# Kernel tuning notes

Measured on AMD Instinct MI355X. Metric: run time of the kernel, lower is better.

The kernel has to match this reference:

```python
import jax, jax.numpy as jnp
import numpy as np

HEAD = 64            # RWKV_HEAD_SIZE
C = 1024             # n_embd = dim_att
F = 4096             # dim_ffn
B, T = 8, 256
H = C // HEAD
N_LAYER, LAYER_ID = 12, 1
GN_EPS = 1e-5 * 8 ** 2   # GroupNorm eps = 1e-5 * head_size_divisor^2


def bshift(x):
    """bidirectional_shift_multihead: per head, first half of channels shifted
    forward in time (right), second half shifted backward (left), zero-padded."""
    b, t, c = x.shape
    x4 = x.reshape(b, t, c // HEAD, HEAD)
    mid = HEAD // 2
    f = jnp.pad(x4[:, :-1, :, :mid], ((0, 0), (1, 0), (0, 0), (0, 0)))
    r = jnp.pad(x4[:, 1:, :, mid:], ((0, 0), (0, 1), (0, 0), (0, 0)))
    return jnp.concatenate([f, r], -1).reshape(b, t, c)


def layernorm(x, g, b):
    m = jnp.mean(x, -1, keepdims=True)
    v = jnp.mean((x - m) ** 2, -1, keepdims=True)
    return (x - m) * jax.lax.rsqrt(v + 1e-5) * g + b


def groupnorm(x, g, b):
    bb, t, c = x.shape
    xg = x.reshape(bb, t, H, HEAD)
    m = jnp.mean(xg, -1, keepdims=True)
    v = jnp.mean((xg - m) ** 2, -1, keepdims=True)
    return ((xg - m) * jax.lax.rsqrt(v + GN_EPS)).reshape(bb, t, c) * g + b


def wkv6_bi(r, k, v, w, u):
    """Bidirectional WKV6. r,k,v,w: [B,T,H,N]; u: [H,N].
    y_t = r_t . (S^fwd_t + u*k_t v_t^T + S^bwd_t), with per-channel decay
    d_t = exp(-exp(w_t)) applied to the state after each step in each direction."""
    d = jnp.exp(-jnp.exp(w))
    rT, kT, vT, dT = (jnp.moveaxis(a, 1, 0) for a in (r, k, v, d))  # [T,B,H,N]
    S0 = jnp.zeros((B, H, HEAD, HEAD), r.dtype)
    uB = u[None]  # [1,H,N]

    def fstep(S, inp):
        rt, kt, vt, dt = inp
        kv = kt[..., None] * vt[..., None, :]              # [B,H,N,N]
        y = jnp.einsum('bhj,bhji->bhi', rt, S + uB[..., None] * kv)
        return dt[..., None] * S + kv, y

    _, yf = jax.lax.scan(fstep, S0, (rT, kT, vT, dT))

    def bstep(S, inp):
        rt, kt, vt, dt = inp
        y = jnp.einsum('bhj,bhji->bhi', rt, S)
        return dt[..., None] * S + kt[..., None] * vt[..., None, :], y

    _, yb = jax.lax.scan(bstep, S0, (rT, kT, vT, dT), reverse=True)
    return jnp.moveaxis(yf + yb, 0, 1)  # [B,T,H,N]


def block_forward(x, ln1_g, ln1_b, ln2_g, ln2_b,
                  maa_x, maa_w, maa_k, maa_v, maa_r, maa_g, maa_w1, maa_w2,
                  time_decay, tdw1, tdw2, u, Wr, Wk, Wv, Wg, Wo, lnx_g, lnx_b,
                  cmaa_k, cmaa_r, Wck, Wcv, Wcr):
    # ---- RWKV_Tmix_V6 (attention) branch ----
    xa = layernorm(x, ln1_g, ln1_b)
    xx = bshift(xa) - xa
    a = jnp.tanh((xa + xx * maa_x) @ maa_w1).reshape(B, T, 5, -1)   # [B,T,5,32]
    m = jnp.einsum('btfd,fdc->fbtc', a, maa_w2)                      # [5,B,T,C]
    xw = xa + xx * (maa_w + m[0])
    xk = xa + xx * (maa_k + m[1])
    xv = xa + xx * (maa_v + m[2])
    xr = xa + xx * (maa_r + m[3])
    xg = xa + xx * (maa_g + m[4])
    r = (xr @ Wr).reshape(B, T, H, HEAD)
    k = (xk @ Wk).reshape(B, T, H, HEAD)
    v = (xv @ Wv).reshape(B, T, H, HEAD)
    g = jax.nn.silu(xg @ Wg)
    w = (time_decay + jnp.tanh(xw @ tdw1) @ tdw2).reshape(B, T, H, HEAD)
    y = wkv6_bi(r, k, v, w, u).reshape(B, T, C)
    y = groupnorm(y, lnx_g, lnx_b)
    x = x + (y * g) @ Wo
    # ---- RWKV_CMix_V6 (FFN) branch ----
    xc = layernorm(x, ln2_g, ln2_b)
    cxx = bshift(xc) - xc
    kk = jnp.square(jax.nn.relu((xc + cxx * cmaa_k) @ Wck))
    kv = kk @ Wcv
    x = x + jax.nn.sigmoid((xc + cxx * cmaa_r) @ Wcr) * kv
    return x


def setup_inputs() -> dict:
    key = jax.random.key(0)
    ks = jax.random.split(key, 16)
    r1 = 1.0 - LAYER_ID / N_LAYER            # ratio_1_to_almost0
    r0 = LAYER_ID / (N_LAYER - 1)            # ratio_0_to_1
    ddd = np.arange(C, dtype=np.float64) / C
    base = (1.0 - ddd ** r1).astype(np.float32)
    half = (1.0 - ddd ** (0.5 * r1)).astype(np.float32)
    s = 0.02
    p = {}
    p['x'] = jax.random.normal(ks[0], (B, T, C), jnp.float32)
    p['ln1_g'] = jnp.ones((C,), jnp.float32)
    p['ln1_b'] = jnp.zeros((C,), jnp.float32)
    p['ln2_g'] = jnp.ones((C,), jnp.float32)
    p['ln2_b'] = jnp.zeros((C,), jnp.float32)
    p['maa_x'] = jnp.asarray(base)
    p['maa_w'] = jnp.asarray(base)
    p['maa_k'] = jnp.asarray(base)
    p['maa_v'] = jnp.asarray((1.0 - (ddd ** r1 + 0.3 * r0)).astype(np.float32))
    p['maa_r'] = jnp.asarray(half)
    p['maa_g'] = jnp.asarray(half)
    p['maa_w1'] = jax.random.uniform(ks[1], (C, 160), jnp.float32, -0.01, 0.01)
    p['maa_w2'] = jax.random.uniform(ks[2], (5, 32, C), jnp.float32, -0.01, 0.01)
    n = np.arange(C, dtype=np.float64)
    p['time_decay'] = jnp.asarray((-6.0 + 5.0 * (n / (C - 1)) ** (0.7 + 1.3 * r0)).astype(np.float32))
    p['tdw1'] = jax.random.uniform(ks[3], (C, 64), jnp.float32, -0.01, 0.01)
    p['tdw2'] = jax.random.uniform(ks[4], (64, C), jnp.float32, -0.01, 0.01)
    faaaa = r0 * (1.0 - n / (C - 1)) + ((n + 1) % 3 - 1) * 0.1
    p['u'] = jnp.asarray(faaaa.reshape(H, HEAD).astype(np.float32))
    p['Wr'] = jax.random.normal(ks[5], (C, C), jnp.float32) * s
    p['Wk'] = jax.random.normal(ks[6], (C, C), jnp.float32) * s
    p['Wv'] = jax.random.normal(ks[7], (C, C), jnp.float32) * s
    p['Wg'] = jax.random.normal(ks[8], (C, C), jnp.float32) * s
    p['Wo'] = jax.random.normal(ks[9], (C, C), jnp.float32) * s
    p['lnx_g'] = jnp.ones((C,), jnp.float32)
    p['lnx_b'] = jnp.zeros((C,), jnp.float32)
    p['cmaa_k'] = jnp.asarray(base)
    p['cmaa_r'] = jnp.asarray(base)
    p['Wck'] = jax.random.normal(ks[10], (C, F), jnp.float32) * s
    p['Wcv'] = jax.random.normal(ks[11], (F, C), jnp.float32) * s
    p['Wcr'] = jax.random.normal(ks[12], (C, C), jnp.float32) * s
    return p


def reference(x, ln1_g, ln1_b, ln2_g, ln2_b,
              maa_x, maa_w, maa_k, maa_v, maa_r, maa_g, maa_w1, maa_w2,
              time_decay, tdw1, tdw2, u, Wr, Wk, Wv, Wg, Wo, lnx_g, lnx_b,
              cmaa_k, cmaa_r, Wck, Wcv, Wcr):
    return block_forward(x, ln1_g, ln1_b, ln2_g, ln2_b,
                         maa_x, maa_w, maa_k, maa_v, maa_r, maa_g, maa_w1, maa_w2,
                         time_decay, tdw1, tdw2, u, Wr, Wk, Wv, Wg, Wo, lnx_g, lnx_b,
                         cmaa_k, cmaa_r, Wck, Wcv, Wcr)
```

## Files before the change

### kernel.cpp

```cpp
#include <hip/hip_runtime.h>
#include <math.h>
#include <stdint.h>

static constexpr int B  = 8;
static constexpr int T  = 256;
static constexpr int C  = 1024;
static constexpr int H  = 16;
static constexpr int HEAD = 64;
static constexpr int FF = 4096;
static constexpr int BT = B * T;
static constexpr int NCH = 8;
static constexpr int CS  = 32;

typedef short short8  __attribute__((ext_vector_type(8)));
typedef float floatx4 __attribute__((ext_vector_type(4)));

__device__ __forceinline__ float bf2f(ushort u) {
    return __uint_as_float(((uint32_t)u) << 16);
}
__device__ __forceinline__ ushort f2bf(float x) {
    uint32_t u = __float_as_uint(x);
    u += 0x7fff + ((u >> 16) & 1);
    return (ushort)(u >> 16);
}

__device__ __forceinline__ void gload16(const void* g, void* l) {
    __builtin_amdgcn_global_load_lds(
        (const __attribute__((address_space(1))) unsigned int*)g,
        (__attribute__((address_space(3))) unsigned int*)l, 16, 0, 0);
}

#define BEPI_NONE_BF   0
#define BEPI_SILU_BF   1
#define BEPI_RELUSQ_BF 2
#define BEPI_NONE_F    3
#define BEPI_RES_F     4
#define BEPI_SIGRES_F  5
#define BEPI_TANH_F    6
#define BEPI_TANH_BF   7
#define BEPI_DECAY_F   8
#define BEPI_SIGRES2_F 9

__device__ __forceinline__ void red6(float (&vals)[6], float* red)
{
    const int wave = threadIdx.x >> 6, lane = threadIdx.x & 63;
#pragma unroll
    for (int i = 0; i < 6; ++i) {
        float v = vals[i];
#pragma unroll
        for (int off = 32; off > 0; off >>= 1) v += __shfl_xor(v, off);
        if (lane == 0) red[i * 4 + wave] = v;
    }
    __syncthreads();
#pragma unroll
    for (int i = 0; i < 6; ++i)
        vals[i] = red[i * 4 + 0] + red[i * 4 + 1] + red[i * 4 + 2] + red[i * 4 + 3];
}

__global__ __launch_bounds__(256) void lnshiftmix_kernel(const float* __restrict__ x,
                                                         const float* __restrict__ g,
                                                         const float* __restrict__ b,
                                                         const float* __restrict__ maa,
                                                         float* __restrict__ xa,
                                                         float* __restrict__ xx,
                                                         ushort* __restrict__ ax)
{
    const int row = blockIdx.x;
    const int t = row & (T - 1);
    const int tid = threadIdx.x;
    __shared__ float red[24];
    const float4 vc = reinterpret_cast<const float4*>(x + (size_t)row * C)[tid];
    float4 vp = make_float4(0.f, 0.f, 0.f, 0.f), vn = make_float4(0.f, 0.f, 0.f, 0.f);
    if (t > 0)     vp = reinterpret_cast<const float4*>(x + (size_t)(row - 1) * C)[tid];
    if (t < T - 1) vn = reinterpret_cast<const float4*>(x + (size_t)(row + 1) * C)[tid];
    float vals[6];
    vals[0] = vc.x + vc.y + vc.z + vc.w;
    vals[1] = vc.x * vc.x + vc.y * vc.y + vc.z * vc.z + vc.w * vc.w;
    vals[2] = vp.x + vp.y + vp.z + vp.w;
    vals[3] = vp.x * vp.x + vp.y * vp.y + vp.z * vp.z + vp.w * vp.w;
    vals[4] = vn.x + vn.y + vn.z + vn.w;
    vals[5] = vn.x * vn.x + vn.y * vn.y + vn.z * vn.z + vn.w * vn.w;
    red6(vals, red);
    const float mc = vals[0] * (1.f / C);
    const float rc = rsqrtf(fmaxf(vals[1] * (1.f / C) - mc * mc, 0.f) + 1e-5f);
    const float mp = vals[2] * (1.f / C);
    const float rp = rsqrtf(fmaxf(vals[3] * (1.f / C) - mp * mp, 0.f) + 1e-5f);
    const float mn = vals[4] * (1.f / C);
    const float rn = rsqrtf(fmaxf(vals[5] * (1.f / C) - mn * mn, 0.f) + 1e-5f);

    const int c = tid * 4;
    const bool fh = ((c & 63) < 32);
    const float cur[4] = {vc.x, vc.y, vc.z, vc.w};
    const float nbr[4] = {fh ? vp.x : vn.x, fh ? vp.y : vn.y,
                          fh ? vp.z : vn.z, fh ? vp.w : vn.w};
    const float mN = fh ? mp : mn, rN = fh ? rp : rn;
    const bool nvalid = fh ? (t > 0) : (t < T - 1);
    const size_t rb = (size_t)row * C;
#pragma unroll
    for (int e = 0; e < 4; ++e) {
        const float gg = g[c + e], bb = b[c + e];
        const float av = (cur[e] - mc) * rc * gg + bb;
        const float sv = nvalid ? ((nbr[e] - mN) * rN * gg + bb) : 0.f;
        const float xv = sv - av;
        xa[rb + c + e] = av;
        xx[rb + c + e] = xv;
        ax[rb + c + e] = f2bf(av + xv * maa[c + e]);
    }
}

__global__ __launch_bounds__(256) void lnshiftcmix_kernel(const float* __restrict__ x,
                                                          const float* __restrict__ g,
                                                          const float* __restrict__ b,
                                                          const float* __restrict__ mk,
                                                          const float* __restrict__ mr,
                                                          ushort* __restrict__ ok,
                                                          ushort* __restrict__ orr)
{
    const int row = blockIdx.x;
    const int t = row & (T - 1);
    const int tid = threadIdx.x;
    __shared__ float red[24];
    const float4 vc = reinterpret_cast<const float4*>(x + (size_t)row * C)[tid];
    float4 vp = make_float4(0.f, 0.f, 0.f, 0.f), vn = make_float4(0.f, 0.f, 0.f, 0.f);
    if (t > 0)     vp = reinterpret_cast<const float4*>(x + (size_t)(row - 1) * C)[tid];
    if (t < T - 1) vn = reinterpret_cast<const float4*>(x + (size_t)(row + 1) * C)[tid];
    float vals[6];
    vals[0] = vc.x + vc.y + vc.z + vc.w;
    vals[1] = vc.x * vc.x + vc.y * vc.y + vc.z * vc.z + vc.w * vc.w;
    vals[2] = vp.x + vp.y + vp.z + vp.w;
    vals[3] = vp.x * vp.x + vp.y * vp.y + vp.z * vp.z + vp.w * vp.w;
    vals[4] = vn.x + vn.y + vn.z + vn.w;
    vals[5] = vn.x * vn.x + vn.y * vn.y + vn.z * vn.z + vn.w * vn.w;
    red6(vals, red);
    const float mc = vals[0] * (1.f / C);
    const float rc = rsqrtf(fmaxf(vals[1] * (1.f / C) - mc * mc, 0.f) + 1e-5f);
    const float mp = vals[2] * (1.f / C);
    const float rp = rsqrtf(fmaxf(vals[3] * (1.f / C) - mp * mp, 0.f) + 1e-5f);
    const float mn = vals[4] * (1.f / C);
    const float rn = rsqrtf(fmaxf(vals[5] * (1.f / C) - mn * mn, 0.f) + 1e-5f);

    const int c = tid * 4;
    const bool fh = ((c & 63) < 32);
    const float cur[4] = {vc.x, vc.y, vc.z, vc.w};
    const float nbr[4] = {fh ? vp.x : vn.x, fh ? vp.y : vn.y,
                          fh ? vp.z : vn.z, fh ? vp.w : vn.w};
    const float mN = fh ? mp : mn, rN = fh ? rp : rn;
    const bool nvalid = fh ? (t > 0) : (t < T - 1);
    const size_t rb = (size_t)row * C;
#pragma unroll
    for (int e = 0; e < 4; ++e) {
        const float gg = g[c + e], bb = b[c + e];
        const float av = (cur[e] - mc) * rc * gg + bb;
        const float sv = nvalid ? ((nbr[e] - mN) * rN * gg + bb) : 0.f;
        const float xv = sv - av;
        ok[rb + c + e]  = f2bf(av + xv * mk[c + e]);
        orr[rb + c + e] = f2bf(av + xv * mr[c + e]);
    }
}

__global__ __launch_bounds__(1024) void gnmul_kernel(const ushort* __restrict__ yf,
                                                     const ushort* __restrict__ yb,
                                                     const float* __restrict__ g,
                                                     const float* __restrict__ b,
                                                     const ushort* __restrict__ gate,
                                                     const ushort* __restrict__ vin,
                                                     const ushort* __restrict__ rbuf,
                                                     const ushort* __restrict__ kbuf,
                                                     const float* __restrict__ u,
                                                     ushort* __restrict__ out)
{
    const int row = blockIdx.x;
    const int tid = threadIdx.x;
    const size_t idx = (size_t)row * C + tid;
    float p = bf2f(rbuf[idx]) * bf2f(kbuf[idx]) * u[tid];
#pragma unroll
    for (int off = 32; off > 0; off >>= 1) p += __shfl_xor(p, off);
    const float v = bf2f(yf[idx]) + bf2f(yb[idx]) + p * bf2f(vin[idx]);
    float s = v;
#pragma unroll
    for (int off = 32; off > 0; off >>= 1) s += __shfl_xor(s, off);
    const float m = s * (1.0f / HEAD);
    const float d = v - m;
    float q = d * d;
#pragma unroll
    for (int off = 32; off > 0; off >>= 1) q += __shfl_xor(q, off);
    const float rstd = rsqrtf(q * (1.0f / HEAD) + 6.4e-4f);
    out[idx] = f2bf((d * rstd * g[tid] + b[tid]) * bf2f(gate[idx]));
}

struct WJobs {
    const float* W[8];
    ushort* dst[8];
    int Kd[8], Nd[8], ntx[8], base[8];
    int njobs;
};
__global__ __launch_bounds__(256) void wconvB_kernel(WJobs jobs)
{
    __shared__ float tile[32][33];
    const int bid = blockIdx.x;
    int j = 0;
#pragma unroll
    for (int i = 1; i < 8; ++i)
        if (i < jobs.njobs && bid >= jobs.base[i]) j = i;
    const float* __restrict__ W = jobs.W[j];
    ushort* __restrict__ dst = jobs.dst[j];
    const int Kd = jobs.Kd[j], Nd = jobs.Nd[j];
    const int local = bid - jobs.base[j];
    const int n0 = (local % jobs.ntx[j]) * 32;
    const int k0 = (local / jobs.ntx[j]) * 32;
    const int tx = threadIdx.x, ty = threadIdx.y;
#pragma unroll
    for (int i = 0; i < 4; ++i)
        tile[ty * 4 + i][tx] = W[(size_t)(k0 + ty * 4 + i) * Nd + n0 + tx];
    __syncthreads();
#pragma unroll
    for (int i = 0; i < 4; ++i)
        dst[(size_t)(n0 + ty * 4 + i) * Kd + k0 + tx] = f2bf(tile[tx][ty * 4 + i]);
}

__global__ __launch_bounds__(256) void wconv_kernel(const float* __restrict__ W,
                                                    ushort* __restrict__ Wt,
                                                    int Kd, int Nd)
{
    __shared__ float tile[32][33];
    const int n0 = blockIdx.x * 32, k0 = blockIdx.y * 32;
    const int tx = threadIdx.x, ty = threadIdx.y;
#pragma unroll
    for (int i = 0; i < 4; ++i)
        tile[ty * 4 + i][tx] = W[(size_t)(k0 + ty * 4 + i) * Nd + n0 + tx];
    __syncthreads();
#pragma unroll
    for (int i = 0; i < 4; ++i)
        Wt[(size_t)(n0 + ty * 4 + i) * Kd + k0 + tx] = f2bf(tile[tx][ty * 4 + i]);
}

struct Wconv4Args { const float* W[4]; };
__global__ __launch_bounds__(256) void wconv4_kernel(Wconv4Args args, ushort* __restrict__ Wt)
{
    __shared__ float tile[32][33];
    const int z = blockIdx.z;
    const float* __restrict__ W = args.W[z];
    ushort* __restrict__ dst = Wt + (size_t)z * C * C;
    const int n0 = blockIdx.x * 32, k0 = blockIdx.y * 32;
    const int tx = threadIdx.x, ty = threadIdx.y;
#pragma unroll
    for (int i = 0; i < 4; ++i)
        tile[ty * 4 + i][tx] = W[(size_t)(k0 + ty * 4 + i) * C + n0 + tx];
    __syncthreads();
#pragma unroll
    for (int i = 0; i < 4; ++i)
        dst[(size_t)(n0 + ty * 4 + i) * C + k0 + tx] = f2bf(tile[tx][ty * 4 + i]);
}

struct Mix5Args { const float* maa[5]; ushort* out[5]; };
__global__ __launch_bounds__(256) void mix5m_kernel(const ushort* __restrict__ a5b,
                                                    const ushort* __restrict__ w2t,
                                                    const float* __restrict__ xa,
                                                    const float* __restrict__ xx,
                                                    Mix5Args args)
{
    __shared__ __align__(16) ushort As[128 * 32];
    __shared__ __align__(16) ushort Bs[64 * 32];
    const int f = blockIdx.z;
    const int bm = blockIdx.y * 128, bn = blockIdx.x * 64;
    const int tid = threadIdx.x;
    const int wid = tid >> 6, lane = tid & 63;
    const int wr = wid >> 1, wc = wid & 1;
    const int l15 = lane & 15, lhi = lane >> 4;

#pragma unroll
    for (int p = 0; p < 2; ++p) {
        const int lin = p * 256 + tid;
        const int row = lin >> 2;
        const int sp = (lin & 3) ^ ((row >> 1) & 3);
        gload16(a5b + (size_t)(bm + row) * 160 + f * 32 + sp * 8, &As[lin * 8]);
    }
    {
        const int lin = tid;
        const int n = lin >> 2;
        const int sp = (lin & 3) ^ ((n >> 1) & 3);
        gload16(w2t + ((size_t)f * C + bn + n) * 32 + sp * 8, &Bs[lin * 8]);
    }
    __syncthreads();

    short8 af[4], bfr[2];
#pragma unroll
    for (int m = 0; m < 4; ++m) {
        const int row = wr * 64 + m * 16 + l15;
        const int sp = lhi ^ ((row >> 1) & 3);
        af[m] = *(const short8*)&As[row * 32 + sp * 8];
    }
#pragma unroll
    for (int n = 0; n < 2; ++n) {
        const int col = wc * 32 + n * 16 + l15;
        const int sp = lhi ^ ((col >> 1) & 3);
        bfr[n] = *(const short8*)&Bs[col * 32 + sp * 8];
    }
    floatx4 acc[4][2];
#pragma unroll
    for (int m = 0; m < 4; ++m)
#pragma unroll
        for (int n = 0; n < 2; ++n)
            acc[m][n] = __builtin_amdgcn_mfma_f32_16x16x32_bf16(
                af[m], bfr[n], (floatx4){0.f, 0.f, 0.f, 0.f}, 0, 0, 0);

    const float* __restrict__ maa = args.maa[f];
    ushort* __restrict__ out = args.out[f];
#pragma unroll
    for (int m = 0; m < 4; ++m) {
        const int row0 = bm + wr * 64 + m * 16 + lhi * 4;
#pragma unroll
        for (int n = 0; n < 2; ++n) {
            const int col = bn + wc * 32 + n * 16 + l15;
            const float mc = maa[col];
#pragma unroll
            for (int j = 0; j < 4; ++j) {
                const size_t oi = (size_t)(row0 + j) * C + col;
                out[oi] = f2bf(xa[oi] + xx[oi] * (mc + acc[m][n][j]));
            }
        }
    }
}

__global__ __launch_bounds__(256) void wkv_pass1(const ushort* __restrict__ k,
                                                 const ushort* __restrict__ v,
                                                 const float* __restrict__ d,
                                                 ushort* __restrict__ M,
                                                 float* __restrict__ D)
{
    const int uc = blockIdx.x;
    const int c = uc & (NCH - 1), unit = uc >> 3;
    const int dir = unit & 1, bh = unit >> 1;
    const int tid = threadIdx.x;
    const int wv = tid >> 6, lane = tid & 63;
    const int l15 = lane & 15, lhi = lane >> 4;
    const size_t rowb = ((size_t)(bh >> 4) * T * H + (bh & 15)) * HEAD;
    const int s0 = c * CS;

    __shared__ ushort kT[64][40];
    __shared__ ushort vt[64][40];
    __shared__ float  Ldd[CS][64];

    for (int idx = tid; idx < CS * 64; idx += 256) {
        const int s = idx >> 6, j = idx & 63;
        const int t = dir ? (T - 1 - (s0 + s)) : (s0 + s);
        const size_t g = rowb + (size_t)t * (H * HEAD) + j;
        kT[j][s] = k[g];
        vt[j][s] = v[g];
        Ldd[s][j] = d[g];
    }
    __syncthreads();

    if (tid < 64) {
        const int j = tid;
        float G = 1.f;
#pragma unroll
        for (int s = CS - 1; s >= 0; --s) {
            kT[j][s] = f2bf(bf2f(kT[j][s]) * G);
            G *= Ldd[s][j];
        }
        D[(size_t)uc * 64 + j] = G;
    }
    __syncthreads();

    const short8 av = *(const short8*)&vt[wv * 16 + l15][lhi * 8];
    ushort* __restrict__ mrow = M + (size_t)uc * 4096;
#pragma unroll
    for (int n = 0; n < 4; ++n) {
        const short8 bk = *(const short8*)&kT[n * 16 + l15][lhi * 8];
        const floatx4 acc = __builtin_amdgcn_mfma_f32_16x16x32_bf16(
            av, bk, (floatx4){0.f, 0.f, 0.f, 0.f}, 0, 0, 0);
#pragma unroll
        for (int jr = 0; jr < 4; ++jr) {
            const int i = wv * 16 + lhi * 4 + jr;
            mrow[(size_t)i * 64 + n * 16 + l15] = f2bf(acc[jr]);
        }
    }
}

__global__ __launch_bounds__(1024) void wkv_pass2(ushort* __restrict__ M,
                                                  const float* __restrict__ D)
{
    const int unit = blockIdx.x;
    const int tid = threadIdx.x;
    const int j0 = (tid & 15) * 4;
    float S0 = 0.f, S1 = 0.f, S2 = 0.f, S3 = 0.f;
#pragma unroll
    for (int c = 0; c < NCH; ++c) {
        const int uc = unit * NCH + c;
        const float4 Dv = *reinterpret_cast<const float4*>(D + (size_t)uc * 64 + j0);
        ushort* mp = M + (size_t)uc * 4096 + tid * 4;
        const uint2 mv = *reinterpret_cast<const uint2*>(mp);
        const float m0 = bf2f((ushort)(mv.x & 0xffff));
        const float m1 = bf2f((ushort)(mv.x >> 16));
        const float m2 = bf2f((ushort)(mv.y & 0xffff));
        const float m3 = bf2f((ushort)(mv.y >> 16));
        uint2 sv;
        sv.x = (uint32_t)f2bf(S0) | ((uint32_t)f2bf(S1) << 16);
        sv.y = (uint32_t)f2bf(S2) | ((uint32_t)f2bf(S3) << 16);
        *reinterpret_cast<uint2*>(mp) = sv;
        S0 = fmaf(Dv.x, S0, m0);
        S1 = fmaf(Dv.y, S1, m1);
        S2 = fmaf(Dv.z, S2, m2);
        S3 = fmaf(Dv.w, S3, m3);
    }
}

__global__ __launch_bounds__(256) void wkv_ymfma(const ushort* __restrict__ r,
                                                 const ushort* __restrict__ k,
                                                 const ushort* __restrict__ v,
                                                 const float* __restrict__ d,
                                                 const ushort* __restrict__ Sin,
                                                 ushort* __restrict__ yf,
                                                 ushort* __restrict__ yb)
{
    const int uc = blockIdx.x;
    const int c = uc & (NCH - 1), unit = uc >> 3;
    const int dir = unit & 1, bh = unit >> 1;
    const int tid = threadIdx.x;
    const int wv = tid >> 6, lane = tid & 63;
    const int l15 = lane & 15, lhi = lane >> 4;
    const size_t rowb = ((size_t)(bh >> 4) * T * H + (bh & 15)) * HEAD;
    const int s0 = c * CS;

    __shared__ ushort rp[32][64];
    __shared__ ushort kp[32][64];
    __shared__ ushort vt[64][40];
    __shared__ ushort Pl[32][32];
    __shared__ float  Ldd[CS][64];

    for (int idx = tid; idx < 32 * 64; idx += 256) {
        const int s = idx >> 6, j = idx & 63;
        const int t = dir ? (T - 1 - (s0 + s)) : (s0 + s);
        const size_t g = rowb + (size_t)t * (H * HEAD) + j;
        const int cs = (j >> 3) ^ (s & 7);
        rp[s][cs * 8 + (j & 7)] = r[g];
        kp[s][cs * 8 + (j & 7)] = k[g];
        vt[j][s] = v[g];
        Ldd[s][j] = d[g];
    }
    __syncthreads();

    if (wv == 0) {
        const int j = lane;
        float Q = 1.f;
#pragma unroll
        for (int s = 0; s < 32; ++s) {
            const int a = ((j >> 3) ^ (s & 7)) * 8 + (j & 7);
            rp[s][a] = f2bf(bf2f(rp[s][a]) * Q);
            Q *= Ldd[s][j];
        }
    } else if (wv == 1) {
        const int j = lane;
        float iQ = 1.f;
#pragma unroll
        for (int s = 0; s < 32; ++s) {
            iQ *= (1.0f / Ldd[s][j]);
            const int a = ((j >> 3) ^ (s & 7)) * 8 + (j & 7);
            kp[s][a] = f2bf(bf2f(kp[s][a]) * iQ);
        }
    }
    __syncthreads();

    const int st = wv & 1;
    const int ip = wv >> 1;

    short8 ar[2];
#pragma unroll
    for (int ks = 0; ks < 2; ++ks) {
        const int row = st * 16 + l15;
        const int ch = (ks * 4 + lhi) ^ (row & 7);
        ar[ks] = *(const short8*)&rp[row][ch * 8];
    }

    floatx4 acc[2];
#pragma unroll
    for (int n = 0; n < 2; ++n) {
        const int i = ip * 32 + n * 16 + l15;
        const ushort* sp = Sin + (size_t)uc * 4096 + (size_t)i * 64;
        const short8 b0 = *(const short8*)&sp[lhi * 8];
        const short8 b1 = *(const short8*)&sp[32 + lhi * 8];
        acc[n] = __builtin_amdgcn_mfma_f32_16x16x32_bf16(ar[0], b0, (floatx4){0.f, 0.f, 0.f, 0.f}, 0, 0, 0);
        acc[n] = __builtin_amdgcn_mfma_f32_16x16x32_bf16(ar[1], b1, acc[n], 0, 0, 0);
    }

    if (wv < 2) {
#pragma unroll
        for (int ut = 0; ut < 2; ++ut) {
            const int urow = ut * 16 + l15;
            const short8 bk0 = *(const short8*)&kp[urow][((0 + lhi) ^ (urow & 7)) * 8];
            const short8 bk1 = *(const short8*)&kp[urow][((4 + lhi) ^ (urow & 7)) * 8];
            floatx4 pa = __builtin_amdgcn_mfma_f32_16x16x32_bf16(ar[0], bk0, (floatx4){0.f, 0.f, 0.f, 0.f}, 0, 0, 0);
            pa = __builtin_amdgcn_mfma_f32_16x16x32_bf16(ar[1], bk1, pa, 0, 0, 0);
            const int sg0 = st * 16 + lhi * 4;
            const int ug = ut * 16 + l15;
#pragma unroll
            for (int jr = 0; jr < 4; ++jr) {
                const float val = (ug < sg0 + jr) ? pa[jr] : 0.f;
                Pl[sg0 + jr][ug] = f2bf(val);
            }
        }
    }
    __syncthreads();

    short8 ap;
    {
        const int row = st * 16 + l15;
        ap = *(const short8*)&Pl[row][lhi * 8];
    }
#pragma unroll
    for (int n = 0; n < 2; ++n) {
        const int i = ip * 32 + n * 16 + l15;
        const short8 bv = *(const short8*)&vt[i][lhi * 8];
        acc[n] = __builtin_amdgcn_mfma_f32_16x16x32_bf16(ap, bv, acc[n], 0, 0, 0);
    }

    ushort* __restrict__ yo = dir ? yb : yf;
#pragma unroll
    for (int n = 0; n < 2; ++n) {
        const int i = ip * 32 + n * 16 + l15;
#pragma unroll
        for (int jr = 0; jr < 4; ++jr) {
            const int sg = st * 16 + lhi * 4 + jr;
            const int t = dir ? (T - 1 - (s0 + sg)) : (s0 + sg);
            yo[rowb + (size_t)t * (H * HEAD) + i] = f2bf(acc[n][jr]);
        }
    }
}

template <int BN>
struct GemmLds {
    ushort As[2][128 * 64];
    ushort Bs[2][BN * 64];
};

template <int BN>
__device__ __forceinline__ void gemm_body8(const ushort* __restrict__ A,
                                           const ushort* __restrict__ Bt,
                                           int bm, int bn, int K, int lda, int ldb,
                                           GemmLds<BN>& lds,
                                           floatx4 (&acc)[4][BN / 64])
{
    constexpr int NF = BN / 64;
    const int tid = threadIdx.x;
    const int wid = tid >> 6, lane = tid & 63;
    const int wr = wid >> 2, wc = wid & 3;
    const int l15 = lane & 15, lhi = lane >> 4;
    const int NT = K >> 6;

    auto stage = [&](int buf, int k0) {
#pragma unroll
        for (int p = 0; p < 2; ++p) {
            const int lin = p * 512 + tid;
            const int row = lin >> 3;
            const int cs = (lin & 7) ^ (row & 7);
            gload16(A + (size_t)(bm + row) * lda + k0 + cs * 8, &lds.As[buf][lin * 8]);
        }
#pragma unroll
        for (int p = 0; p < NF; ++p) {
            const int lin = p * 512 + tid;
            const int n = lin >> 3;
            const int cs = (lin & 7) ^ (n & 7);
            gload16(Bt + (size_t)(bn + n) * ldb + k0 + cs * 8, &lds.Bs[buf][lin * 8]);
        }
    };

    stage(0, 0);
    __syncthreads();
    for (int t = 0; t < NT; ++t) {
        const int cur = t & 1;
        if (t + 1 < NT) stage(cur ^ 1, (t + 1) << 6);

        short8 af[4][2];
#pragma unroll
        for (int m = 0; m < 4; ++m) {
            const int row = wr * 64 + m * 16 + l15;
#pragma unroll
            for (int s = 0; s < 2; ++s) {
                const int cc = (s * 4 + lhi) ^ (row & 7);
                af[m][s] = *(const short8*)&lds.As[cur][row * 64 + cc * 8];
            }
        }
        short8 bf[NF][2];
#pragma unroll
        for (int n = 0; n < NF; ++n) {
            const int col = wc * (BN / 4) + n * 16 + l15;
#pragma unroll
            for (int s = 0; s < 2; ++s) {
                const int cc = (s * 4 + lhi) ^ (col & 7);
                bf[n][s] = *(const short8*)&lds.Bs[cur][col * 64 + cc * 8];
            }
        }
#pragma unroll
        for (int m = 0; m < 4; ++m)
#pragma unroll
            for (int n = 0; n < NF; ++n) {
                acc[m][n] = __builtin_amdgcn_mfma_f32_16x16x32_bf16(af[m][0], bf[n][0], acc[m][n], 0, 0, 0);
                acc[m][n] = __builtin_amdgcn_mfma_f32_16x16x32_bf16(af[m][1], bf[n][1], acc[m][n], 0, 0, 0);
            }
        __syncthreads();
    }
}

template <int BN, int EPI>
__global__ __launch_bounds__(512) void bgemm_kernel(const ushort* __restrict__ A,
                                                    const ushort* __restrict__ Bt,
                                                    void* __restrict__ Cm,
                                                    int M, int N, int K,
                                                    const float* __restrict__ aux1,
                                                    const float* __restrict__ aux2,
                                                    const float* __restrict__ aux3)
{
    constexpr int NF = BN / 64;
    __shared__ GemmLds<BN> lds;
    int w = blockIdx.y * gridDim.x + blockIdx.x;
    const int nwg = gridDim.x * gridDim.y;
    if ((nwg & 7) == 0) w = (w & 7) * (nwg >> 3) + (w >> 3);
    const int bn = (w % gridDim.x) * BN;
    const int bm = (w / gridDim.x) * 128;
    const int tid = threadIdx.x;
    const int wid = tid >> 6, lane = tid & 63;
    const int wr = wid >> 2, wc = wid & 3;
    const int l15 = lane & 15, lhi = lane >> 4;

    floatx4 acc[4][NF];
#pragma unroll
    for (int m = 0; m < 4; ++m)
#pragma unroll
        for (int n = 0; n < NF; ++n) acc[m][n] = (floatx4){0.f, 0.f, 0.f, 0.f};

    gemm_body8<BN>(A, Bt, bm, bn, K, K, K, lds, acc);

#pragma unroll
    for (int m = 0; m < 4; ++m) {
        const int row0 = bm + wr * 64 + m * 16 + lhi * 4;
#pragma unroll
        for (int n = 0; n < NF; ++n) {
            const int col = bn + wc * (BN / 4) + n * 16 + l15;
            if (col >= N) continue;
#pragma unroll
            for (int j = 0; j < 4; ++j) {
                const size_t oi = (size_t)(row0 + j) * N + col;
                const float a = acc[m][n][j];
                if constexpr (EPI == BEPI_NONE_BF) {
                    ((ushort*)Cm)[oi] = f2bf(a);
                } else if constexpr (EPI == BEPI_SILU_BF) {
                    ((ushort*)Cm)[oi] = f2bf(a / (1.f + __expf(-a)));
                } else if constexpr (EPI == BEPI_RELUSQ_BF) {
                    const float t = fmaxf(a, 0.f);
                    ((ushort*)Cm)[oi] = f2bf(t * t);
                } else if constexpr (EPI == BEPI_NONE_F) {
                    ((float*)Cm)[oi] = a;
                } else if constexpr (EPI == BEPI_RES_F) {
                    ((float*)Cm)[oi] = aux1[oi] + a;
                } else if constexpr (EPI == BEPI_SIGRES_F) {
                    ((float*)Cm)[oi] = aux1[oi] + aux2[oi] / (1.f + __expf(-a));
                } else if constexpr (EPI == BEPI_SIGRES2_F) {
                    const float kv = bf2f(((const ushort*)aux2)[oi]) +
                                     bf2f(((const ushort*)aux3)[oi]);
                    ((float*)Cm)[oi] = aux1[oi] + kv / (1.f + __expf(-a));
                } else if constexpr (EPI == BEPI_TANH_F) {
                    ((float*)Cm)[oi] = tanhf(a);
                } else if constexpr (EPI == BEPI_TANH_BF) {
                    ((ushort*)Cm)[oi] = f2bf(tanhf(a));
                } else {
                    ((float*)Cm)[oi] = __expf(-__expf(a + aux1[col]));
                }
            }
        }
    }
}

__global__ __launch_bounds__(512) void wcv_kernel(const ushort* __restrict__ A,
                                                  const ushort* __restrict__ Bt,
                                                  ushort* __restrict__ P0,
                                                  ushort* __restrict__ P1)
{
    __shared__ GemmLds<64> lds;
    const int z = blockIdx.z;
    int w = blockIdx.y * gridDim.x + blockIdx.x;
    w = (w & 7) * 32 + (w >> 3);
    const int bn = (w % 16) * 64;
    const int bm = (w / 16) * 128;
    const int tid = threadIdx.x;
    const int wid = tid >> 6, lane = tid & 63;
    const int wr = wid >> 2, wc = wid & 3;
    const int l15 = lane & 15, lhi = lane >> 4;

    floatx4 acc[4][1];
#pragma unroll
    for (int m = 0; m < 4; ++m) acc[m][0] = (floatx4){0.f, 0.f, 0.f, 0.f};

    gemm_body8<64>(A + z * (FF / 2), Bt + z * (FF / 2), bm, bn, FF / 2, FF, FF, lds, acc);

    ushort* __restrict__ P = z ? P1 : P0;
#pragma unroll
    for (int m = 0; m < 4; ++m) {
        const int row0 = bm + wr * 64 + m * 16 + lhi * 4;
        const int col = bn + wc * 16 + l15;
#pragma unroll
        for (int j = 0; j < 4; ++j)
            P[(size_t)(row0 + j) * C + col] = f2bf(acc[m][0][j]);
    }
}

struct QkvgArgs { const ushort* A[4]; ushort* O[4]; };
__global__ __launch_bounds__(512) void qkvg_kernel(QkvgArgs args,
                                                   const ushort* __restrict__ Wt)
{
    __shared__ GemmLds<128> lds;
    const int z = blockIdx.z;
    int w = blockIdx.y * gridDim.x + blockIdx.x;
    w = (w & 7) * 16 + (w >> 3);
    const int bn = (w & 7) * 128;
    const int bm = (w >> 3) * 128;
    const int tid = threadIdx.x;
    const int wid = tid >> 6, lane = tid & 63;
    const int wr = wid >> 2, wc = wid & 3;
    const int l15 = lane & 15, lhi = lane >> 4;

    floatx4 acc[4][2];
#pragma unroll
    for (int m = 0; m < 4; ++m)
#pragma unroll
        for (int n = 0; n < 2; ++n) acc[m][n] = (floatx4){0.f, 0.f, 0.f, 0.f};

    gemm_body8<128>(args.A[z], Wt + (size_t)z * C * C, bm, bn, C, C, C, lds, acc);

    ushort* __restrict__ O = args.O[z];
    const bool silu = (z == 3);
#pragma unroll
    for (int m = 0; m < 4; ++m) {
        const int row0 = bm + wr * 64 + m * 16 + lhi * 4;
#pragma unroll
        for (int n = 0; n < 2; ++n) {
            const int col = bn + wc * 32 + n * 16 + l15;
#pragma unroll
            for (int j = 0; j < 4; ++j) {
                float a = acc[m][n][j];
                if (silu) a = a / (1.f + __expf(-a));
                O[(size_t)(row0 + j) * C + col] = f2bf(a);
            }
        }
    }
}

extern "C" void kernel_launch(void* const* d_in, const int* in_sizes, int n_in,
                              void* d_out, int out_size, void* d_ws, size_t ws_size,
                              hipStream_t stream)
{
    const float* x        = (const float*)d_in[0];
    const float* ln1_g    = (const float*)d_in[1];
    const float* ln1_b    = (const float*)d_in[2];
    const float* ln2_g    = (const float*)d_in[3];
    const float* ln2_b    = (const float*)d_in[4];
    const float* maa_x    = (const float*)d_in[5];
    const float* maa_w    = (const float*)d_in[6];
    const float* maa_k    = (const float*)d_in[7];
    const float* maa_v    = (const float*)d_in[8];
    const float* maa_r    = (const float*)d_in[9];
    const float* maa_g    = (const float*)d_in[10];
    const float* maa_w1   = (const float*)d_in[11];
    const float* maa_w2   = (const float*)d_in[12];
    const float* time_dec = (const float*)d_in[13];
    const float* tdw1     = (const float*)d_in[14];
    const float* tdw2     = (const float*)d_in[15];
    const float* u        = (const float*)d_in[16];
    const float* Wr       = (const float*)d_in[17];
    const float* Wk       = (const float*)d_in[18];
    const float* Wv       = (const float*)d_in[19];
    const float* Wg       = (const float*)d_in[20];
    const float* Wo       = (const float*)d_in[21];
    const float* lnx_g    = (const float*)d_in[22];
    const float* lnx_b    = (const float*)d_in[23];
    const float* cmaa_k   = (const float*)d_in[24];
    const float* cmaa_r   = (const float*)d_in[25];
    const float* Wck      = (const float*)d_in[26];
    const float* Wcv      = (const float*)d_in[27];
    const float* Wcr      = (const float*)d_in[28];
    float* out = (float*)d_out;

    float* fws = (float*)d_ws;
    const size_t E = (size_t)BT * C;
    float* xa  = fws + 0 * E;
    float* xx  = fws + 1 * E;
    float* wd  = fws + 2 * E;
    float* fs  = fws + 3 * E;
    ushort* wBuf = (ushort*)(fws + 4 * E);
    ushort* Mbuf = (ushort*)fs;
    ushort* w2t  = wBuf + (size_t)C * 160;
    ushort* t1wt = wBuf + (size_t)C * 320;
    ushort* t2wt = wBuf + (size_t)C * 384;
    ushort* bf1  = wBuf + (size_t)C * FF;
    ushort* rb   = bf1 + E;
    ushort* kb   = rb + E;
    ushort* vb   = kb + E;
    ushort* gb   = vb + E;
    ushort* t1b  = gb + E;
    float* a5    = (float*)(t1b + (size_t)BT * 64);
    float* sig   = a5 + (size_t)BT * 160;
    float* Dbuf  = sig + (size_t)BT * H;
    ushort* a5b  = (ushort*)a5;
    ushort* xvb  = (ushort*)fs;
    ushort* xrb  = (ushort*)fs + E;
    ushort* xgb  = (ushort*)out;
    ushort* xwb  = (ushort*)out + E;
    ushort* yfb  = (ushort*)xa;
    ushort* ybb  = (ushort*)xa + E;
    ushort* p0b  = (ushort*)fs;
    ushort* p1b  = (ushort*)fs + E;
    ushort* kk   = (ushort*)xa;

    const dim3 blk(256);
    const dim3 gblk(512);
    const dim3 tblk(32, 8);
    const dim3 gNN(C / 64, BT / 128);

    WJobs ej;
    ej.njobs = 8;
    ej.W[0] = maa_w1; ej.dst[0] = wBuf; ej.Kd[0] = C; ej.Nd[0] = 160; ej.ntx[0] = 5; ej.base[0] = 0;
    for (int f = 0; f < 5; ++f) {
        ej.W[1 + f] = maa_w2 + (size_t)f * 32 * C;
        ej.dst[1 + f] = w2t + (size_t)f * C * 32;
        ej.Kd[1 + f] = 32; ej.Nd[1 + f] = C; ej.ntx[1 + f] = 32;
        ej.base[1 + f] = 160 + f * 32;
    }
    ej.W[6] = tdw1; ej.dst[6] = t1wt; ej.Kd[6] = C; ej.Nd[6] = 64; ej.ntx[6] = 2; ej.base[6] = 320;
    ej.W[7] = tdw2; ej.dst[7] = t2wt; ej.Kd[7] = 64; ej.Nd[7] = C; ej.ntx[7] = 32; ej.base[7] = 384;
    wconvB_kernel<<<dim3(448), tblk, 0, stream>>>(ej);

    lnshiftmix_kernel<<<BT, blk, 0, stream>>>(x, ln1_g, ln1_b, maa_x, xa, xx, bf1);
    bgemm_kernel<64, BEPI_TANH_BF><<<dim3(3, BT / 128), gblk, 0, stream>>>(bf1, wBuf, a5b, BT, 160, C, nullptr, nullptr, nullptr);

    Mix5Args margs;
    margs.maa[0] = maa_w; margs.maa[1] = maa_k; margs.maa[2] = maa_v;
    margs.maa[3] = maa_r; margs.maa[4] = maa_g;
    margs.out[0] = xwb; margs.out[1] = bf1; margs.out[2] = xvb;
    margs.out[3] = xrb; margs.out[4] = xgb;
    mix5m_kernel<<<dim3(C / 64, BT / 128, 5), blk, 0, stream>>>(a5b, w2t, xa, xx, margs);

    bgemm_kernel<64, BEPI_TANH_BF><<<dim3(1, BT / 128), gblk, 0, stream>>>(xwb, t1wt, t1b, BT, 64, C, nullptr, nullptr, nullptr);
    bgemm_kernel<64, BEPI_DECAY_F><<<gNN, gblk, 0, stream>>>(t1b, t2wt, wd, BT, C, 64, time_dec, nullptr, nullptr);

    Wconv4Args wargs;
    wargs.W[0] = Wk; wargs.W[1] = Wv; wargs.W[2] = Wr; wargs.W[3] = Wg;
    wconv4_kernel<<<dim3(C / 32, C / 32, 4), tblk, 0, stream>>>(wargs, wBuf);
    QkvgArgs qargs;
    qargs.A[0] = bf1; qargs.A[1] = xvb; qargs.A[2] = xrb; qargs.A[3] = xgb;
    qargs.O[0] = kb;  qargs.O[1] = vb;  qargs.O[2] = rb;  qargs.O[3] = gb;
    qkvg_kernel<<<dim3(8, 16, 4), gblk, 0, stream>>>(qargs, wBuf);

    wkv_pass1<<<dim3(2 * B * H * NCH), blk, 0, stream>>>(kb, vb, wd, Mbuf, Dbuf);
    wkv_pass2<<<dim3(2 * B * H), dim3(1024), 0, stream>>>(Mbuf, Dbuf);
    wkv_ymfma<<<dim3(2 * B * H * NCH), blk, 0, stream>>>(rb, kb, vb, wd, Mbuf, yfb, ybb);

    gnmul_kernel<<<BT, dim3(1024), 0, stream>>>(yfb, ybb, lnx_g, lnx_b, gb, vb, rb, kb, u, vb);
    wconv_kernel<<<dim3(C / 32, C / 32), tblk, 0, stream>>>(Wo, wBuf, C, C);
    bgemm_kernel<64, BEPI_RES_F><<<gNN, gblk, 0, stream>>>(vb, wBuf, out, BT, C, C, x, nullptr, nullptr);

    lnshiftcmix_kernel<<<BT, blk, 0, stream>>>(out, ln2_g, ln2_b, cmaa_k, cmaa_r, bf1, gb);
    wconv_kernel<<<dim3(FF / 32, C / 32), tblk, 0, stream>>>(Wck, wBuf, C, FF);
    bgemm_kernel<128, BEPI_RELUSQ_BF><<<dim3(FF / 128, BT / 128), gblk, 0, stream>>>(bf1, wBuf, kk, BT, FF, C, nullptr, nullptr, nullptr);

    WJobs fj;
    fj.njobs = 2;
    fj.W[0] = Wcv; fj.dst[0] = wBuf; fj.Kd[0] = FF; fj.Nd[0] = C; fj.ntx[0] = 32; fj.base[0] = 0;
    fj.W[1] = Wcr; fj.dst[1] = rb;   fj.Kd[1] = C;  fj.Nd[1] = C; fj.ntx[1] = 32; fj.base[1] = 4096;
    for (int i = 2; i < 8; ++i) { fj.W[i] = nullptr; fj.dst[i] = nullptr; fj.Kd[i] = 1; fj.Nd[i] = 1; fj.ntx[i] = 1; fj.base[i] = 1 << 30; }
    wconvB_kernel<<<dim3(4096 + 1024), tblk, 0, stream>>>(fj);

    wcv_kernel<<<dim3(16, 16, 2), gblk, 0, stream>>>(kk, wBuf, p0b, p1b);
    bgemm_kernel<64, BEPI_SIGRES2_F><<<gNN, gblk, 0, stream>>>(gb, rb, out, BT, C, C, out, (const float*)p0b, (const float*)p1b);

    (void)in_sizes; (void)n_in; (void)out_size; (void)ws_size;
}
```

Before: 233.8 us.

## Store LN mix intermediates as bf16, batch weight conversions, prefetch wkv pass2 loads

```diff
diff --git a/kernel.cpp b/kernel.cpp
--- a/kernel.cpp
+++ b/kernel.cpp
@@ -61,8 +61,8 @@
                                                          const float* __restrict__ g,
                                                          const float* __restrict__ b,
                                                          const float* __restrict__ maa,
-                                                         float* __restrict__ xa,
-                                                         float* __restrict__ xx,
+                                                         ushort* __restrict__ xa,
+                                                         ushort* __restrict__ xx,
                                                          ushort* __restrict__ ax)
 {
     const int row = blockIdx.x;
@@ -102,8 +102,8 @@
         const float av = (cur[e] - mc) * rc * gg + bb;
         const float sv = nvalid ? ((nbr[e] - mN) * rN * gg + bb) : 0.f;
         const float xv = sv - av;
-        xa[rb + c + e] = av;
-        xx[rb + c + e] = xv;
+        xa[rb + c + e] = f2bf(av);
+        xx[rb + c + e] = f2bf(xv);
         ax[rb + c + e] = f2bf(av + xv * maa[c + e]);
     }
 }
@@ -218,22 +218,6 @@
         dst[(size_t)(n0 + ty * 4 + i) * Kd + k0 + tx] = f2bf(tile[tx][ty * 4 + i]);
 }
 
-__global__ __launch_bounds__(256) void wconv_kernel(const float* __restrict__ W,
-                                                    ushort* __restrict__ Wt,
-                                                    int Kd, int Nd)
-{
-    __shared__ float tile[32][33];
-    const int n0 = blockIdx.x * 32, k0 = blockIdx.y * 32;
-    const int tx = threadIdx.x, ty = threadIdx.y;
-#pragma unroll
-    for (int i = 0; i < 4; ++i)
-        tile[ty * 4 + i][tx] = W[(size_t)(k0 + ty * 4 + i) * Nd + n0 + tx];
-    __syncthreads();
-#pragma unroll
-    for (int i = 0; i < 4; ++i)
-        Wt[(size_t)(n0 + ty * 4 + i) * Kd + k0 + tx] = f2bf(tile[tx][ty * 4 + i]);
-}
-
 struct Wconv4Args { const float* W[4]; };
 __global__ __launch_bounds__(256) void wconv4_kernel(Wconv4Args args, ushort* __restrict__ Wt)
 {
@@ -255,8 +239,8 @@
 struct Mix5Args { const float* maa[5]; ushort* out[5]; };
 __global__ __launch_bounds__(256) void mix5m_kernel(const ushort* __restrict__ a5b,
                                                     const ushort* __restrict__ w2t,
-                                                    const float* __restrict__ xa,
-                                                    const float* __restrict__ xx,
+                                                    const ushort* __restrict__ xa,
+                                                    const ushort* __restrict__ xx,
                                                     Mix5Args args)
 {
     __shared__ __align__(16) ushort As[128 * 32];
@@ -316,7 +300,7 @@
 #pragma unroll
             for (int j = 0; j < 4; ++j) {
                 const size_t oi = (size_t)(row0 + j) * C + col;
-                out[oi] = f2bf(xa[oi] + xx[oi] * (mc + acc[m][n][j]));
+                out[oi] = f2bf(bf2f(xa[oi]) + bf2f(xx[oi]) * (mc + acc[m][n][j]));
             }
         }
     }
@@ -384,25 +368,26 @@
     const int unit = blockIdx.x;
     const int tid = threadIdx.x;
     const int j0 = (tid & 15) * 4;
-    float S0 = 0.f, S1 = 0.f, S2 = 0.f, S3 = 0.f;
+    uint2 mv[NCH];
+    float4 Dv[NCH];
 #pragma unroll
     for (int c = 0; c < NCH; ++c) {
         const int uc = unit * NCH + c;
-        const float4 Dv = *reinterpret_cast<const float4*>(D + (size_t)uc * 64 + j0);
-        ushort* mp = M + (size_t)uc * 4096 + tid * 4;
-        const uint2 mv = *reinterpret_cast<const uint2*>(mp);
-        const float m0 = bf2f((ushort)(mv.x & 0xffff));
-        const float m1 = bf2f((ushort)(mv.x >> 16));
-        const float m2 = bf2f((ushort)(mv.y & 0xffff));
-        const float m3 = bf2f((ushort)(mv.y >> 16));
+        mv[c] = *reinterpret_cast<const uint2*>(M + (size_t)uc * 4096 + tid * 4);
+        Dv[c] = *reinterpret_cast<const float4*>(D + (size_t)uc * 64 + j0);
+    }
+    float S0 = 0.f, S1 = 0.f, S2 = 0.f, S3 = 0.f;
+#pragma unroll
+    for (int c = 0; c < NCH; ++c) {
+        const int uc = unit * NCH + c;
         uint2 sv;
         sv.x = (uint32_t)f2bf(S0) | ((uint32_t)f2bf(S1) << 16);
         sv.y = (uint32_t)f2bf(S2) | ((uint32_t)f2bf(S3) << 16);
-        *reinterpret_cast<uint2*>(mp) = sv;
-        S0 = fmaf(Dv.x, S0, m0);
-        S1 = fmaf(Dv.y, S1, m1);
-        S2 = fmaf(Dv.z, S2, m2);
-        S3 = fmaf(Dv.w, S3, m3);
+        *reinterpret_cast<uint2*>(M + (size_t)uc * 4096 + tid * 4) = sv;
+        S0 = fmaf(Dv[c].x, S0, bf2f((ushort)(mv[c].x & 0xffff)));
+        S1 = fmaf(Dv[c].y, S1, bf2f((ushort)(mv[c].x >> 16)));
+        S2 = fmaf(Dv[c].z, S2, bf2f((ushort)(mv[c].y & 0xffff)));
+        S3 = fmaf(Dv[c].w, S3, bf2f((ushort)(mv[c].y >> 16)));
     }
 }
 
@@ -805,11 +790,14 @@
     ushort* xrb  = (ushort*)fs + E;
     ushort* xgb  = (ushort*)out;
     ushort* xwb  = (ushort*)out + E;
+    ushort* xab  = (ushort*)xa;
+    ushort* xxb  = (ushort*)xa + E;
     ushort* yfb  = (ushort*)xa;
     ushort* ybb  = (ushort*)xa + E;
     ushort* p0b  = (ushort*)fs;
     ushort* p1b  = (ushort*)fs + E;
     ushort* kk   = (ushort*)xa;
+    ushort* wcvb = (ushort*)wd;
 
     const dim3 blk(256);
     const dim3 gblk(512);
@@ -829,7 +817,7 @@
     ej.W[7] = tdw2; ej.dst[7] = t2wt; ej.Kd[7] = 64; ej.Nd[7] = C; ej.ntx[7] = 32; ej.base[7] = 384;
     wconvB_kernel<<<dim3(448), tblk, 0, stream>>>(ej);
 
-    lnshiftmix_kernel<<<BT, blk, 0, stream>>>(x, ln1_g, ln1_b, maa_x, xa, xx, bf1);
+    lnshiftmix_kernel<<<BT, blk, 0, stream>>>(x, ln1_g, ln1_b, maa_x, xab, xxb, bf1);
     bgemm_kernel<64, BEPI_TANH_BF><<<dim3(3, BT / 128), gblk, 0, stream>>>(bf1, wBuf, a5b, BT, 160, C, nullptr, nullptr, nullptr);
 
     Mix5Args margs;
@@ -837,7 +825,7 @@
     margs.maa[3] = maa_r; margs.maa[4] = maa_g;
     margs.out[0] = xwb; margs.out[1] = bf1; margs.out[2] = xvb;
     margs.out[3] = xrb; margs.out[4] = xgb;
-    mix5m_kernel<<<dim3(C / 64, BT / 128, 5), blk, 0, stream>>>(a5b, w2t, xa, xx, margs);
+    mix5m_kernel<<<dim3(C / 64, BT / 128, 5), blk, 0, stream>>>(a5b, w2t, xab, xxb, margs);
 
     bgemm_kernel<64, BEPI_TANH_BF><<<dim3(1, BT / 128), gblk, 0, stream>>>(xwb, t1wt, t1b, BT, 64, C, nullptr, nullptr, nullptr);
     bgemm_kernel<64, BEPI_DECAY_F><<<gNN, gblk, 0, stream>>>(t1b, t2wt, wd, BT, C, 64, time_dec, nullptr, nullptr);
@@ -855,21 +843,21 @@
     wkv_ymfma<<<dim3(2 * B * H * NCH), blk, 0, stream>>>(rb, kb, vb, wd, Mbuf, yfb, ybb);
 
     gnmul_kernel<<<BT, dim3(1024), 0, stream>>>(yfb, ybb, lnx_g, lnx_b, gb, vb, rb, kb, u, vb);
-    wconv_kernel<<<dim3(C / 32, C / 32), tblk, 0, stream>>>(Wo, wBuf, C, C);
-    bgemm_kernel<64, BEPI_RES_F><<<gNN, gblk, 0, stream>>>(vb, wBuf, out, BT, C, C, x, nullptr, nullptr);
+
+    WJobs mj;
+    mj.njobs = 4;
+    mj.W[0] = Wo;  mj.dst[0] = kb;   mj.Kd[0] = C;  mj.Nd[0] = C;  mj.ntx[0] = 32;  mj.base[0] = 0;
+    mj.W[1] = Wck; mj.dst[1] = wBuf; mj.Kd[1] = C;  mj.Nd[1] = FF; mj.ntx[1] = 128; mj.base[1] = 1024;
+    mj.W[2] = Wcv; mj.dst[2] = wcvb; mj.Kd[2] = FF; mj.Nd[2] = C;  mj.ntx[2] = 32;  mj.base[2] = 5120;
+    mj.W[3] = Wcr; mj.dst[3] = rb;   mj.Kd[3] = C;  mj.Nd[3] = C;  mj.ntx[3] = 32;  mj.base[3] = 9216;
+    for (int i = 4; i < 8; ++i) { mj.W[i] = nullptr; mj.dst[i] = nullptr; mj.Kd[i] = 1; mj.Nd[i] = 1; mj.ntx[i] = 1; mj.base[i] = 1 << 30; }
+    wconvB_kernel<<<dim3(10240), tblk, 0, stream>>>(mj);
+
+    bgemm_kernel<64, BEPI_RES_F><<<gNN, gblk, 0, stream>>>(vb, kb, out, BT, C, C, x, nullptr, nullptr);
 
     lnshiftcmix_kernel<<<BT, blk, 0, stream>>>(out, ln2_g, ln2_b, cmaa_k, cmaa_r, bf1, gb);
-    wconv_kernel<<<dim3(FF / 32, C / 32), tblk, 0, stream>>>(Wck, wBuf, C, FF);
     bgemm_kernel<128, BEPI_RELUSQ_BF><<<dim3(FF / 128, BT / 128), gblk, 0, stream>>>(bf1, wBuf, kk, BT, FF, C, nullptr, nullptr, nullptr);
-
-    WJobs fj;
-    fj.njobs = 2;
-    fj.W[0] = Wcv; fj.dst[0] = wBuf; fj.Kd[0] = FF; fj.Nd[0] = C; fj.ntx[0] = 32; fj.base[0] = 0;
-    fj.W[1] = Wcr; fj.dst[1] = rb;   fj.Kd[1] = C;  fj.Nd[1] = C; fj.ntx[1] = 32; fj.base[1] = 4096;
-    for (int i = 2; i < 8; ++i) { fj.W[i] = nullptr; fj.dst[i] = nullptr; fj.Kd[i] = 1; fj.Nd[i] = 1; fj.ntx[i] = 1; fj.base[i] = 1 << 30; }
-    wconvB_kernel<<<dim3(4096 + 1024), tblk, 0, stream>>>(fj);
-
-    wcv_kernel<<<dim3(16, 16, 2), gblk, 0, stream>>>(kk, wBuf, p0b, p1b);
+    wcv_kernel<<<dim3(16, 16, 2), gblk, 0, stream>>>(kk, wcvb, p0b, p1b);
     bgemm_kernel<64, BEPI_SIGRES2_F><<<gNN, gblk, 0, stream>>>(gb, rb, out, BT, C, C, out, (const float*)p0b, (const float*)p1b);
 
     (void)in_sizes; (void)n_in; (void)out_size; (void)ws_size;
```

Result: no change. 233.5 us (median of 2 runs) (-0.1%).
